# Performance work log

Hardware: AMD Instinct MI355X
Metric: run time of the kernel (lower is better)

Reference implementation:

```python
import jax, jax.numpy as jnp
import numpy as np

D_MODEL = 768
NUM_HEADS = 12


def setup_inputs() -> dict:
    key = jax.random.key(0)
    ks = jax.random.split(key, 11)
    B, N, D = 4, 2048, D_MODEL
    s = 1.0 / np.sqrt(D)
    return {
        "q": jax.random.normal(ks[0], (B, N, D), jnp.float32),
        "k": jax.random.normal(ks[1], (B, N, D), jnp.float32),
        "v": jax.random.normal(ks[2], (B, N, D), jnp.float32),
        "wq": jax.random.normal(ks[3], (D, D), jnp.float32) * s,
        "bq": jnp.zeros((D,), jnp.float32),
        "wk": jax.random.normal(ks[4], (D, D), jnp.float32) * s,
        "bk": jnp.zeros((D,), jnp.float32),
        "wv": jax.random.normal(ks[5], (D, D), jnp.float32) * s,
        "bv": jnp.zeros((D,), jnp.float32),
        "wo": jax.random.normal(ks[6], (D, D), jnp.float32) * s,
        "bo": jnp.zeros((D,), jnp.float32),
    }


def _split_heads(x, num_heads):
    B, N, D = x.shape
    hd = D // num_heads
    return x.reshape(B, N, num_heads, hd).transpose(0, 2, 1, 3)  # (B,H,N,hd)


def reference(q, k, v, wq, bq, wk, bk, wv, bv, wo, bo):
    B, N, D = q.shape
    H = NUM_HEADS
    qw = q @ wq.T + bq
    kw = k @ wk.T + bk
    vw = v @ wv.T + bv
    hq = _split_heads(qw, H)
    hk = _split_heads(kw, H)
    hv = _split_heads(vw, H)
    scale = 1.0 / jnp.sqrt(jnp.asarray(hq.shape[-1], hq.dtype))
    scores = jnp.einsum("bhnd,bhmd->bhnm", hq, hk) * scale  # (B,H,N,N) explicit
    attn = jax.nn.softmax(scores, axis=-1)
    out = jnp.einsum("bhnm,bhmd->bhnd", attn, hv)
    out = out.transpose(0, 2, 1, 3).reshape(B, N, D)
    return out @ wo.T + bo
```

## Files before the change

kernel.cpp:

```cpp
#include <hip/hip_runtime.h>
#include <hip/hip_bf16.h>
#include <type_traits>


typedef __attribute__((ext_vector_type(8)))  __bf16 bf16x8;
typedef __attribute__((ext_vector_type(4)))  __bf16 bf16x4;
typedef __attribute__((ext_vector_type(4)))  float  f32x4;
typedef __attribute__((ext_vector_type(16))) float  f32x16;
typedef __attribute__((ext_vector_type(2)))  unsigned u32x2;
typedef __attribute__((ext_vector_type(4)))  unsigned u32x4;

#define NH  12
#define HD  64
#define DM  768
#define SEQ 2048
#define NB  4
#define M8  8192
#define ALPHA 0.18033688011112043f

__device__ __forceinline__ f32x4 mfma16(bf16x8 a, bf16x8 b, f32x4 c) {
  return __builtin_amdgcn_mfma_f32_16x16x32_bf16(a, b, c, 0, 0, 0);
}
__device__ __forceinline__ f32x16 mfma32(bf16x8 a, bf16x8 b, f32x16 c) {
  return __builtin_amdgcn_mfma_f32_32x32x16_bf16(a, b, c, 0, 0, 0);
}
__device__ __forceinline__ void gload16(const void* g, void* l) {
  auto gp = (__attribute__((address_space(1))) void*)(const_cast<void*>(g));
  auto lp = (__attribute__((address_space(3))) void*)(l);
  __builtin_amdgcn_global_load_lds(gp, lp, 16, 0, 0);
}
__device__ __forceinline__ float exp2_(float x) {
#if __has_builtin(__builtin_amdgcn_exp2f)
  return __builtin_amdgcn_exp2f(x);
#else
  return exp2f(x);
#endif
}

__device__ __forceinline__ u32x2 pswap(unsigned a, unsigned b) {
#if __has_builtin(__builtin_amdgcn_permlane32_swap)
  return __builtin_amdgcn_permlane32_swap(a, b, false, false);
#else
  u32x2 r;
  unsigned sa = (unsigned)__shfl_xor((int)a, 32), sb = (unsigned)__shfl_xor((int)b, 32);
  int hi = ((int)threadIdx.x >> 5) & 1;
  r[0] = hi ? sb : a;
  r[1] = hi ? b : sa;
  return r;
#endif
}
__device__ __forceinline__ unsigned f2u(float x) { return __builtin_bit_cast(unsigned, x); }
__device__ __forceinline__ float    u2f(unsigned x) { return __builtin_bit_cast(float, x); }
__device__ __forceinline__ float pcomb_sum(float v) {
  u32x2 r = pswap(f2u(v), f2u(v));
  return u2f(r[0]) + u2f(r[1]);
}
__device__ __forceinline__ unsigned pk(float lo, float hi_) {
  unsigned short ua = __builtin_bit_cast(unsigned short, (__bf16)lo);
  unsigned short ub = __builtin_bit_cast(unsigned short, (__bf16)hi_);
  return ((unsigned)ub << 16) | ua;
}

__global__ void cast3_kernel(const float* __restrict__ a, const float* __restrict__ b,
                             const float* __restrict__ c,
                             __bf16* __restrict__ oa, __bf16* __restrict__ ob,
                             __bf16* __restrict__ oc, int n4) {
  const float* in = blockIdx.y == 0 ? a : blockIdx.y == 1 ? b : c;
  __bf16* out     = blockIdx.y == 0 ? oa : blockIdx.y == 1 ? ob : oc;
  const float sc  = blockIdx.y == 0 ? ALPHA : 1.0f;
  int i = blockIdx.x * 256 + threadIdx.x;
  if (i < n4) {
    float4 v = ((const float4*)in)[i];
    bf16x4 r;
    r[0] = (__bf16)(v.x * sc); r[1] = (__bf16)(v.y * sc);
    r[2] = (__bf16)(v.z * sc); r[3] = (__bf16)(v.w * sc);
    ((bf16x4*)out)[i] = r;
  }
}

__global__ void cast4_kernel(const float* __restrict__ a, const float* __restrict__ b,
                             const float* __restrict__ c, const float* __restrict__ d,
                             __bf16* __restrict__ oa, __bf16* __restrict__ ob,
                             __bf16* __restrict__ oc, __bf16* __restrict__ od, int n4) {
  int y = blockIdx.y;
  const float* in = y == 0 ? a : y == 1 ? b : y == 2 ? c : d;
  __bf16* out     = y == 0 ? oa : y == 1 ? ob : y == 2 ? oc : od;
  int i = blockIdx.x * 256 + threadIdx.x;
  if (i < n4) {
    float4 v = ((const float4*)in)[i];
    bf16x4 r;
    r[0] = (__bf16)v.x; r[1] = (__bf16)v.y; r[2] = (__bf16)v.z; r[3] = (__bf16)v.w;
    ((bf16x4*)out)[i] = r;
  }
}

template <typename OutT>
__device__ __forceinline__ void gemm_body(const __bf16* __restrict__ A,
                                          const __bf16* __restrict__ B,
                                          const float* __restrict__ bias,
                                          OutT* __restrict__ C,
                                          long m0, long n0, float bscale, bool trans) {
  __shared__ __align__(16) __bf16 As[128][32];
  __shared__ __align__(16) __bf16 Bs[128][32];
  const int tid = threadIdx.x;
  const int w = tid >> 6, l = tid & 63;
  const int g = l >> 4, i16 = l & 15;
  const int wr = w >> 1, wc = w & 1;
  const int srow = l >> 2;
  const int scol = (l & 3) * 8;
  f32x4 acc[4][4] = {};

  for (int k0 = 0; k0 < DM; k0 += 32) {
    __syncthreads();
#pragma unroll
    for (int s = 0; s < 2; ++s) {
      const int r0 = (s * 4 + w) * 16;
      gload16(A + (m0 + r0 + srow) * (long)DM + k0 + scol, &As[r0][0]);
      gload16(B + (n0 + r0 + srow) * (long)DM + k0 + scol, &Bs[r0][0]);
    }
    __syncthreads();
    bf16x8 af[4], bfr[4];
#pragma unroll
    for (int m = 0; m < 4; ++m) af[m] = *(const bf16x8*)&As[wr * 64 + m * 16 + i16][g * 8];
#pragma unroll
    for (int n = 0; n < 4; ++n) bfr[n] = *(const bf16x8*)&Bs[wc * 64 + n * 16 + i16][g * 8];
#pragma unroll
    for (int m = 0; m < 4; ++m)
#pragma unroll
      for (int n = 0; n < 4; ++n) acc[m][n] = mfma16(af[m], bfr[n], acc[m][n]);
  }

  if (trans) {
#pragma unroll
    for (int m = 0; m < 4; ++m)
#pragma unroll
      for (int n = 0; n < 4; ++n) {
        const long col = n0 + wc * 64 + n * 16 + i16;
        const float bv = bias[col] * bscale;
        const long row0 = m0 + wr * 64 + m * 16 + g * 4;
        bf16x4 v4;
#pragma unroll
        for (int r = 0; r < 4; ++r) v4[r] = (__bf16)(acc[m][n][r] + bv);
        *(bf16x4*)((__bf16*)C + col * (long)M8 + row0) = v4;
      }
  } else {
#pragma unroll
    for (int m = 0; m < 4; ++m)
#pragma unroll
      for (int n = 0; n < 4; ++n) {
        const long col = n0 + wc * 64 + n * 16 + i16;
        const float bv = bias[col] * bscale;
        const long row0 = m0 + wr * 64 + m * 16 + g * 4;
#pragma unroll
        for (int r = 0; r < 4; ++r) {
          const float v = acc[m][n][r] + bv;
          if constexpr (std::is_same<OutT, float>::value)
            C[(row0 + r) * DM + col] = v;
          else
            C[(row0 + r) * DM + col] = (__bf16)v;
        }
      }
  }
}

__global__ __launch_bounds__(256) void proj3_gemm(
    const __bf16* __restrict__ qb, const __bf16* __restrict__ kb, const __bf16* __restrict__ vb,
    const __bf16* __restrict__ wqb, const __bf16* __restrict__ wkb, const __bf16* __restrict__ wvb,
    const float* __restrict__ bq, const float* __restrict__ bk, const float* __restrict__ bv,
    __bf16* __restrict__ qpj, __bf16* __restrict__ kpj, __bf16* __restrict__ vpT) {
  const int gid = blockIdx.x;
  const int swz = (gid & 7) * 144 + (gid >> 3);
  const int z = swz / 384, rem = swz % 384;
  const long xb = rem / 6, yb = rem % 6;
  const __bf16* A = z == 0 ? qb : z == 1 ? kb : vb;
  const __bf16* B = z == 0 ? wqb : z == 1 ? wkb : wvb;
  const float* bias = z == 0 ? bq : z == 1 ? bk : bv;
  __bf16* C = z == 0 ? qpj : z == 1 ? kpj : vpT;
  gemm_body<__bf16>(A, B, bias, C, xb * 128, yb * 128, z == 0 ? ALPHA : 1.0f, z == 2);
}

__global__ __launch_bounds__(256) void out_gemm(const __bf16* __restrict__ A,
                                                const __bf16* __restrict__ B,
                                                const float* __restrict__ bias,
                                                float* __restrict__ C) {
  const int gid = blockIdx.x;
  const int swz = (gid & 7) * 48 + (gid >> 3);
  const long xb = swz / 6, yb = swz % 6;
  gemm_body<float>(A, B, bias, C, xb * 128, yb * 128, 1.0f, false);
}

__global__ __launch_bounds__(256) void attn_fwd(const __bf16* __restrict__ qp,
                                                const __bf16* __restrict__ kp,
                                                const __bf16* __restrict__ vpT,
                                                __bf16* __restrict__ ao) {
  __shared__ __align__(16) __bf16 Ks[2][64 * 64];
  __shared__ __align__(16) __bf16 Vs[2][64 * 64];

  const int wg = blockIdx.x;
  const int xcd = wg & 7;
  const int idx = wg >> 3;
  const int bh = xcd * 6 + (idx >> 4);
  const int qt = idx & 15;
  const int b = bh / NH, h = bh % NH;

  const int tid = threadIdx.x;
  const int w = tid >> 6, l = tid & 63;
  const int l31 = l & 31, hi = l >> 5;

  const long qrow = (long)b * SEQ + qt * 128 + w * 32 + l31;
  const __bf16* qb = qp + qrow * DM + h * HD;
  bf16x8 qf[4];
#pragma unroll
  for (int kk = 0; kk < 4; ++kk) qf[kk] = *(const bf16x8*)(qb + kk * 16 + hi * 8);

  f32x16 o0 = {}, o1 = {};
  float lsum = 0.f;

  const int srow = tid >> 3;
  const int schunk = (tid & 7) ^ (srow & 7);
  const __bf16* kbase = kp + ((long)b * SEQ) * DM + h * HD;
  const __bf16* vtb = vpT + (long)(h * HD) * M8 + (long)b * SEQ;

  auto stage = [&](int T, int sel) {
    const long kt = (long)T * 64;
    __bf16* Kd = &Ks[sel][(w * 8) * 64];
    __bf16* Vd = &Vs[sel][(w * 8) * 64];
    gload16(kbase + (kt + srow) * (long)DM + schunk * 8, Kd);
    gload16(kbase + (kt + 32 + srow) * (long)DM + schunk * 8, Kd + 32 * 64);
    gload16(vtb + (long)srow * M8 + kt + schunk * 8, Vd);
    gload16(vtb + (long)(32 + srow) * M8 + kt + schunk * 8, Vd + 32 * 64);
  };

  auto compute = [&](const __bf16* Kc, const __bf16* Vc) {
    f32x16 s0 = {}, s1 = {};
    __builtin_amdgcn_s_setprio(1);
#pragma unroll
    for (int kk = 0; kk < 4; ++kk) {
      const int cl = kk * 2 + hi;
      bf16x8 kf0 = *(const bf16x8*)&Kc[l31 * 64 + ((cl ^ (l31 & 7)) * 8)];
      s0 = mfma32(kf0, qf[kk], s0);
      bf16x8 kf1 = *(const bf16x8*)&Kc[(32 + l31) * 64 + ((cl ^ (l31 & 7)) * 8)];
      s1 = mfma32(kf1, qf[kk], s1);
    }
    __builtin_amdgcn_s_setprio(0);

#pragma unroll
    for (int r = 0; r < 16; ++r) s0[r] = exp2_(s0[r]);
#pragma unroll
    for (int r = 0; r < 16; ++r) s1[r] = exp2_(s1[r]);
    f32x16 ps = s0 + s1;
    const float t0 = (ps[0] + ps[1]) + (ps[2] + ps[3]);
    const float t1 = (ps[4] + ps[5]) + (ps[6] + ps[7]);
    const float t2 = (ps[8] + ps[9]) + (ps[10] + ps[11]);
    const float t3 = (ps[12] + ps[13]) + (ps[14] + ps[15]);
    lsum += (t0 + t1) + (t2 + t3);

    bf16x8 pf[4];
#pragma unroll
    for (int ks = 0; ks < 4; ++ks) {
      const int base = 8 * (ks & 1);
      const f32x16& S = (ks < 2) ? s0 : s1;
      unsigned pa = pk(S[base + 0], S[base + 1]);
      unsigned pc = pk(S[base + 2], S[base + 3]);
      unsigned pb = pk(S[base + 4], S[base + 5]);
      unsigned pd = pk(S[base + 6], S[base + 7]);
      u32x2 r02 = pswap(pa, pb);
      u32x2 r13 = pswap(pc, pd);
      u32x4 pw;
      pw[0] = r02[0]; pw[1] = r13[0]; pw[2] = r02[1]; pw[3] = r13[1];
      pf[ks] = __builtin_bit_cast(bf16x8, pw);
    }

    __builtin_amdgcn_s_setprio(1);
#pragma unroll
    for (int ks = 0; ks < 4; ++ks) {
      const int cl = ks * 2 + hi;
      bf16x8 vf0 = *(const bf16x8*)&Vc[l31 * 64 + ((cl ^ (l31 & 7)) * 8)];
      o0 = mfma32(vf0, pf[ks], o0);
      bf16x8 vf1 = *(const bf16x8*)&Vc[(32 + l31) * 64 + ((cl ^ (l31 & 7)) * 8)];
      o1 = mfma32(vf1, pf[ks], o1);
    }
    __builtin_amdgcn_s_setprio(0);
  };

  stage(0, 0);
  __syncthreads();
  for (int t = 0; t < SEQ / 64; t += 2) {
    if (t + 1 < SEQ / 64) stage(t + 1, 1);
    compute(Ks[0], Vs[0]);
    __syncthreads();
    if (t + 2 < SEQ / 64) stage(t + 2, 0);
    compute(Ks[1], Vs[1]);
    __syncthreads();
  }

  const float inv = 1.0f / pcomb_sum(lsum);
  __bf16* obase = ao + qrow * DM + h * HD;
#pragma unroll
  for (int rg = 0; rg < 4; ++rg) {
    bf16x4 v0, v1;
#pragma unroll
    for (int j = 0; j < 4; ++j) {
      v0[j] = (__bf16)(o0[rg * 4 + j] * inv);
      v1[j] = (__bf16)(o1[rg * 4 + j] * inv);
    }
    *(bf16x4*)(obase + 8 * rg + 4 * hi) = v0;
    *(bf16x4*)(obase + 32 + 8 * rg + 4 * hi) = v1;
  }
}

extern "C" void kernel_launch(void* const* d_in, const int* in_sizes, int n_in,
                              void* d_out, int out_size, void* d_ws, size_t ws_size,
                              hipStream_t stream) {
  const float* q  = (const float*)d_in[0];
  const float* k  = (const float*)d_in[1];
  const float* v  = (const float*)d_in[2];
  const float* wq = (const float*)d_in[3];
  const float* bq = (const float*)d_in[4];
  const float* wk = (const float*)d_in[5];
  const float* bk = (const float*)d_in[6];
  const float* wv = (const float*)d_in[7];
  const float* bv = (const float*)d_in[8];
  const float* wo = (const float*)d_in[9];
  const float* bo = (const float*)d_in[10];

  const long S = (long)M8 * DM;
  const long W = (long)DM * DM;
  __bf16* ws = (__bf16*)d_ws;
  __bf16 *qb = ws, *kb = qb + S, *vb = kb + S;
  __bf16 *wqb = vb + S, *wkb = wqb + W, *wvb = wkb + W, *wob = wvb + W;
  __bf16 *qpj = wob + W, *kpj = qpj + S, *vpT = kpj + S;
  __bf16* aob = qb;

  cast3_kernel<<<dim3((unsigned)(S / 4 / 256), 3), 256, 0, stream>>>(q, k, v, qb, kb, vb, (int)(S / 4));
  cast4_kernel<<<dim3((unsigned)(W / 4 / 256), 4), 256, 0, stream>>>(wq, wk, wv, wo, wqb, wkb, wvb, wob, (int)(W / 4));

  proj3_gemm<<<1152, 256, 0, stream>>>(qb, kb, vb, wqb, wkb, wvb, bq, bk, bv, qpj, kpj, vpT);

  attn_fwd<<<768, 256, 0, stream>>>(qpj, kpj, vpT, aob);

  out_gemm<<<384, 256, 0, stream>>>(aob, wob, bo, (float*)d_out);
}
```

Before: 168.8 us.

## Double-buffer GEMM and attention loads with explicit vmcnt waits and swizzled LDS

```diff
diff --git a/kernel.cpp b/kernel.cpp
--- a/kernel.cpp
+++ b/kernel.cpp
@@ -29,13 +29,12 @@
   auto lp = (__attribute__((address_space(3))) void*)(l);
   __builtin_amdgcn_global_load_lds(gp, lp, 16, 0, 0);
 }
-__device__ __forceinline__ float exp2_(float x) {
-#if __has_builtin(__builtin_amdgcn_exp2f)
-  return __builtin_amdgcn_exp2f(x);
-#else
-  return exp2f(x);
-#endif
-}
+__device__ __forceinline__ float exp2_(float x) { return exp2f(x); }
+
+#define VMW(n) do { asm volatile("s_waitcnt vmcnt(" #n ")" ::: "memory"); \
+                    __builtin_amdgcn_sched_barrier(0); } while (0)
+#define BARX do { __builtin_amdgcn_s_barrier(); \
+                  __builtin_amdgcn_sched_barrier(0); } while (0)
 
 __device__ __forceinline__ u32x2 pswap(unsigned a, unsigned b) {
 #if __has_builtin(__builtin_amdgcn_permlane32_swap)
@@ -100,35 +99,51 @@
                                           const float* __restrict__ bias,
                                           OutT* __restrict__ C,
                                           long m0, long n0, float bscale, bool trans) {
-  __shared__ __align__(16) __bf16 As[128][32];
-  __shared__ __align__(16) __bf16 Bs[128][32];
+  __shared__ __align__(16) char LDSG[32768];
   const int tid = threadIdx.x;
   const int w = tid >> 6, l = tid & 63;
   const int g = l >> 4, i16 = l & 15;
   const int wr = w >> 1, wc = w & 1;
   const int srow = l >> 2;
-  const int scol = (l & 3) * 8;
+  const int scol = ((l & 3) ^ ((srow >> 1) & 3)) * 8;
+  const __bf16* Ag0 = A + (m0 + 16 * w + srow) * (long)DM + scol;
+  const __bf16* Bg0 = B + (n0 + 16 * w + srow) * (long)DM + scol;
+  const int chsw = (g ^ ((i16 >> 1) & 3)) * 16;
+  const char* fA = LDSG + (wr * 64 + i16) * 64 + chsw;
+  const char* fB = LDSG + 16384 + (wc * 64 + i16) * 64 + chsw;
+
   f32x4 acc[4][4] = {};
-
-  for (int k0 = 0; k0 < DM; k0 += 32) {
-    __syncthreads();
-#pragma unroll
-    for (int s = 0; s < 2; ++s) {
-      const int r0 = (s * 4 + w) * 16;
-      gload16(A + (m0 + r0 + srow) * (long)DM + k0 + scol, &As[r0][0]);
-      gload16(B + (n0 + r0 + srow) * (long)DM + k0 + scol, &Bs[r0][0]);
-    }
-    __syncthreads();
-    bf16x8 af[4], bfr[4];
-#pragma unroll
-    for (int m = 0; m < 4; ++m) af[m] = *(const bf16x8*)&As[wr * 64 + m * 16 + i16][g * 8];
-#pragma unroll
-    for (int n = 0; n < 4; ++n) bfr[n] = *(const bf16x8*)&Bs[wc * 64 + n * 16 + i16][g * 8];
-#pragma unroll
-    for (int m = 0; m < 4; ++m)
-#pragma unroll
-      for (int n = 0; n < 4; ++n) acc[m][n] = mfma16(af[m], bfr[n], acc[m][n]);
-  }
+  int kcur = 0;
+
+#define GSTAGE(SELB) do { \
+    gload16(Ag0 + kcur, LDSG + (SELB) + w * 1024); \
+    gload16(Ag0 + 64 * (long)DM + kcur, LDSG + (SELB) + w * 1024 + 4096); \
+    gload16(Bg0 + kcur, LDSG + 16384 + (SELB) + w * 1024); \
+    gload16(Bg0 + 64 * (long)DM + kcur, LDSG + 16384 + (SELB) + w * 1024 + 4096); \
+    kcur += 32; } while (0)
+
+#define GCOMPUTE(SELB) do { \
+    bf16x8 af[4], bfr[4]; \
+    _Pragma("unroll") for (int m = 0; m < 4; ++m) \
+      af[m] = *(const bf16x8*)(fA + (SELB) + m * 1024); \
+    _Pragma("unroll") for (int n = 0; n < 4; ++n) \
+      bfr[n] = *(const bf16x8*)(fB + (SELB) + n * 1024); \
+    __builtin_amdgcn_s_setprio(1); \
+    _Pragma("unroll") for (int m = 0; m < 4; ++m) \
+      _Pragma("unroll") for (int n = 0; n < 4; ++n) \
+        acc[m][n] = mfma16(af[m], bfr[n], acc[m][n]); \
+    __builtin_amdgcn_s_setprio(0); } while (0)
+
+  GSTAGE(0); GSTAGE(8192);
+#pragma unroll 1
+  for (int k = 0; k + 128 <= DM; k += 64) {
+    VMW(4); BARX; GCOMPUTE(0);    BARX; GSTAGE(0);
+    VMW(4); BARX; GCOMPUTE(8192); BARX; GSTAGE(8192);
+  }
+  VMW(4); BARX; GCOMPUTE(0);
+  VMW(0); BARX; GCOMPUTE(8192);
+#undef GSTAGE
+#undef GCOMPUTE
 
   if (trans) {
 #pragma unroll
@@ -193,8 +208,7 @@
                                                 const __bf16* __restrict__ kp,
                                                 const __bf16* __restrict__ vpT,
                                                 __bf16* __restrict__ ao) {
-  __shared__ __align__(16) __bf16 Ks[2][64 * 64];
-  __shared__ __align__(16) __bf16 Vs[2][64 * 64];
+  __shared__ __align__(16) __bf16 KV[16384];
 
   const int wg = blockIdx.x;
   const int xcd = wg & 7;
@@ -213,86 +227,78 @@
 #pragma unroll
   for (int kk = 0; kk < 4; ++kk) qf[kk] = *(const bf16x8*)(qb + kk * 16 + hi * 8);
 
+  const char* fb[4];
+#pragma unroll
+  for (int kk = 0; kk < 4; ++kk)
+    fb[kk] = (const char*)KV + l31 * 128 + (((kk * 2 + hi) ^ (l31 & 7)) * 16);
+
   f32x16 o0 = {}, o1 = {};
   float lsum = 0.f;
 
   const int srow = tid >> 3;
   const int schunk = (tid & 7) ^ (srow & 7);
-  const __bf16* kbase = kp + ((long)b * SEQ) * DM + h * HD;
-  const __bf16* vtb = vpT + (long)(h * HD) * M8 + (long)b * SEQ;
-
-  auto stage = [&](int T, int sel) {
-    const long kt = (long)T * 64;
-    __bf16* Kd = &Ks[sel][(w * 8) * 64];
-    __bf16* Vd = &Vs[sel][(w * 8) * 64];
-    gload16(kbase + (kt + srow) * (long)DM + schunk * 8, Kd);
-    gload16(kbase + (kt + 32 + srow) * (long)DM + schunk * 8, Kd + 32 * 64);
-    gload16(vtb + (long)srow * M8 + kt + schunk * 8, Vd);
-    gload16(vtb + (long)(32 + srow) * M8 + kt + schunk * 8, Vd + 32 * 64);
-  };
-
-  auto compute = [&](const __bf16* Kc, const __bf16* Vc) {
-    f32x16 s0 = {}, s1 = {};
-    __builtin_amdgcn_s_setprio(1);
-#pragma unroll
-    for (int kk = 0; kk < 4; ++kk) {
-      const int cl = kk * 2 + hi;
-      bf16x8 kf0 = *(const bf16x8*)&Kc[l31 * 64 + ((cl ^ (l31 & 7)) * 8)];
-      s0 = mfma32(kf0, qf[kk], s0);
-      bf16x8 kf1 = *(const bf16x8*)&Kc[(32 + l31) * 64 + ((cl ^ (l31 & 7)) * 8)];
-      s1 = mfma32(kf1, qf[kk], s1);
-    }
-    __builtin_amdgcn_s_setprio(0);
-
-#pragma unroll
-    for (int r = 0; r < 16; ++r) s0[r] = exp2_(s0[r]);
-#pragma unroll
-    for (int r = 0; r < 16; ++r) s1[r] = exp2_(s1[r]);
-    f32x16 ps = s0 + s1;
-    const float t0 = (ps[0] + ps[1]) + (ps[2] + ps[3]);
-    const float t1 = (ps[4] + ps[5]) + (ps[6] + ps[7]);
-    const float t2 = (ps[8] + ps[9]) + (ps[10] + ps[11]);
-    const float t3 = (ps[12] + ps[13]) + (ps[14] + ps[15]);
-    lsum += (t0 + t1) + (t2 + t3);
-
-    bf16x8 pf[4];
-#pragma unroll
-    for (int ks = 0; ks < 4; ++ks) {
-      const int base = 8 * (ks & 1);
-      const f32x16& S = (ks < 2) ? s0 : s1;
-      unsigned pa = pk(S[base + 0], S[base + 1]);
-      unsigned pc = pk(S[base + 2], S[base + 3]);
-      unsigned pb = pk(S[base + 4], S[base + 5]);
-      unsigned pd = pk(S[base + 6], S[base + 7]);
-      u32x2 r02 = pswap(pa, pb);
-      u32x2 r13 = pswap(pc, pd);
-      u32x4 pw;
-      pw[0] = r02[0]; pw[1] = r13[0]; pw[2] = r02[1]; pw[3] = r13[1];
-      pf[ks] = __builtin_bit_cast(bf16x8, pw);
-    }
-
-    __builtin_amdgcn_s_setprio(1);
-#pragma unroll
-    for (int ks = 0; ks < 4; ++ks) {
-      const int cl = ks * 2 + hi;
-      bf16x8 vf0 = *(const bf16x8*)&Vc[l31 * 64 + ((cl ^ (l31 & 7)) * 8)];
-      o0 = mfma32(vf0, pf[ks], o0);
-      bf16x8 vf1 = *(const bf16x8*)&Vc[(32 + l31) * 64 + ((cl ^ (l31 & 7)) * 8)];
-      o1 = mfma32(vf1, pf[ks], o1);
-    }
-    __builtin_amdgcn_s_setprio(0);
-  };
-
-  stage(0, 0);
-  __syncthreads();
-  for (int t = 0; t < SEQ / 64; t += 2) {
-    if (t + 1 < SEQ / 64) stage(t + 1, 1);
-    compute(Ks[0], Vs[0]);
-    __syncthreads();
-    if (t + 2 < SEQ / 64) stage(t + 2, 0);
-    compute(Ks[1], Vs[1]);
-    __syncthreads();
-  }
+  const __bf16* kg = kp + ((long)b * SEQ + srow) * DM + h * HD + schunk * 8;
+  const __bf16* vg = vpT + ((long)(h * HD) + srow) * M8 + (long)b * SEQ + schunk * 8;
+  char* kdst = (char*)KV + w * 1024;
+
+#define ASTAGE(SELB) do { \
+    gload16(kg, kdst + (SELB)); \
+    gload16(kg + 32 * (long)DM, kdst + (SELB) + 4096); \
+    gload16(vg, kdst + 16384 + (SELB)); \
+    gload16(vg + 32 * (long)M8, kdst + 16384 + (SELB) + 4096); \
+    kg += 64 * (long)DM; vg += 64; } while (0)
+
+#define ACOMPUTE(SELB) do { \
+    f32x16 s0 = {}, s1 = {}; \
+    __builtin_amdgcn_s_setprio(1); \
+    _Pragma("unroll") for (int kk = 0; kk < 4; ++kk) { \
+      bf16x8 kf0 = *(const bf16x8*)(fb[kk] + (SELB)); \
+      s0 = mfma32(kf0, qf[kk], s0); \
+      bf16x8 kf1 = *(const bf16x8*)(fb[kk] + (SELB) + 4096); \
+      s1 = mfma32(kf1, qf[kk], s1); \
+    } \
+    __builtin_amdgcn_s_setprio(0); \
+    _Pragma("unroll") for (int r = 0; r < 16; ++r) s0[r] = exp2_(s0[r]); \
+    _Pragma("unroll") for (int r = 0; r < 16; ++r) s1[r] = exp2_(s1[r]); \
+    f32x16 ps = s0 + s1; \
+    const float t0 = (ps[0] + ps[1]) + (ps[2] + ps[3]); \
+    const float t1 = (ps[4] + ps[5]) + (ps[6] + ps[7]); \
+    const float t2 = (ps[8] + ps[9]) + (ps[10] + ps[11]); \
+    const float t3 = (ps[12] + ps[13]) + (ps[14] + ps[15]); \
+    lsum += (t0 + t1) + (t2 + t3); \
+    bf16x8 pf[4]; \
+    _Pragma("unroll") for (int ks = 0; ks < 4; ++ks) { \
+      const int base = 8 * (ks & 1); \
+      const f32x16& S = (ks < 2) ? s0 : s1; \
+      unsigned pa = pk(S[base + 0], S[base + 1]); \
+      unsigned pc = pk(S[base + 2], S[base + 3]); \
+      unsigned pb = pk(S[base + 4], S[base + 5]); \
+      unsigned pd = pk(S[base + 6], S[base + 7]); \
+      u32x2 r02 = pswap(pa, pb); \
+      u32x2 r13 = pswap(pc, pd); \
+      u32x4 pw; \
+      pw[0] = r02[0]; pw[1] = r13[0]; pw[2] = r02[1]; pw[3] = r13[1]; \
+      pf[ks] = __builtin_bit_cast(bf16x8, pw); \
+    } \
+    __builtin_amdgcn_s_setprio(1); \
+    _Pragma("unroll") for (int ks = 0; ks < 4; ++ks) { \
+      bf16x8 vf0 = *(const bf16x8*)(fb[ks] + 16384 + (SELB)); \
+      o0 = mfma32(vf0, pf[ks], o0); \
+      bf16x8 vf1 = *(const bf16x8*)(fb[ks] + 16384 + (SELB) + 4096); \
+      o1 = mfma32(vf1, pf[ks], o1); \
+    } \
+    __builtin_amdgcn_s_setprio(0); } while (0)
+
+  ASTAGE(0); ASTAGE(8192);
+#pragma unroll 1
+  for (int t = 0; t + 4 <= SEQ / 64; t += 2) {
+    VMW(4); BARX; ACOMPUTE(0);    BARX; ASTAGE(0);
+    VMW(4); BARX; ACOMPUTE(8192); BARX; ASTAGE(8192);
+  }
+  VMW(4); BARX; ACOMPUTE(0);
+  VMW(0); BARX; ACOMPUTE(8192);
+#undef ASTAGE
+#undef ACOMPUTE
 
   const float inv = 1.0f / pcomb_sum(lsum);
   __bf16* obase = ao + qrow * DM + h * HD;
```

New measurement: 189.8 us. 1.12x slower.

## Fuse fp32 activation cast into projection GEMM with double-buffered swizzled LDS

Applied to the files above, without the earlier changes.

```diff
diff --git a/kernel.cpp b/kernel.cpp
--- a/kernel.cpp
+++ b/kernel.cpp
@@ -29,13 +29,7 @@
   auto lp = (__attribute__((address_space(3))) void*)(l);
   __builtin_amdgcn_global_load_lds(gp, lp, 16, 0, 0);
 }
-__device__ __forceinline__ float exp2_(float x) {
-#if __has_builtin(__builtin_amdgcn_exp2f)
-  return __builtin_amdgcn_exp2f(x);
-#else
-  return exp2f(x);
-#endif
-}
+__device__ __forceinline__ float exp2_(float x) { return exp2f(x); }
 
 __device__ __forceinline__ u32x2 pswap(unsigned a, unsigned b) {
 #if __has_builtin(__builtin_amdgcn_permlane32_swap)
@@ -61,13 +55,14 @@
   return ((unsigned)ub << 16) | ua;
 }
 
-__global__ void cast3_kernel(const float* __restrict__ a, const float* __restrict__ b,
-                             const float* __restrict__ c,
+__global__ void cast4_kernel(const float* __restrict__ a, const float* __restrict__ b,
+                             const float* __restrict__ c, const float* __restrict__ d,
                              __bf16* __restrict__ oa, __bf16* __restrict__ ob,
-                             __bf16* __restrict__ oc, int n4) {
-  const float* in = blockIdx.y == 0 ? a : blockIdx.y == 1 ? b : c;
-  __bf16* out     = blockIdx.y == 0 ? oa : blockIdx.y == 1 ? ob : oc;
-  const float sc  = blockIdx.y == 0 ? ALPHA : 1.0f;
+                             __bf16* __restrict__ oc, __bf16* __restrict__ od, int n4) {
+  int y = blockIdx.y;
+  const float* in = y == 0 ? a : y == 1 ? b : y == 2 ? c : d;
+  __bf16* out     = y == 0 ? oa : y == 1 ? ob : y == 2 ? oc : od;
+  const float sc  = y == 0 ? ALPHA : 1.0f;
   int i = blockIdx.x * 256 + threadIdx.x;
   if (i < n4) {
     float4 v = ((const float4*)in)[i];
@@ -78,57 +73,88 @@
   }
 }
 
-__global__ void cast4_kernel(const float* __restrict__ a, const float* __restrict__ b,
-                             const float* __restrict__ c, const float* __restrict__ d,
-                             __bf16* __restrict__ oa, __bf16* __restrict__ ob,
-                             __bf16* __restrict__ oc, __bf16* __restrict__ od, int n4) {
-  int y = blockIdx.y;
-  const float* in = y == 0 ? a : y == 1 ? b : y == 2 ? c : d;
-  __bf16* out     = y == 0 ? oa : y == 1 ? ob : y == 2 ? oc : od;
-  int i = blockIdx.x * 256 + threadIdx.x;
-  if (i < n4) {
-    float4 v = ((const float4*)in)[i];
-    bf16x4 r;
-    r[0] = (__bf16)v.x; r[1] = (__bf16)v.y; r[2] = (__bf16)v.z; r[3] = (__bf16)v.w;
-    ((bf16x4*)out)[i] = r;
-  }
-}
-
-template <typename OutT>
-__device__ __forceinline__ void gemm_body(const __bf16* __restrict__ A,
+template <typename AT, typename OutT>
+__device__ __forceinline__ void gemm_body(const AT* __restrict__ A,
                                           const __bf16* __restrict__ B,
                                           const float* __restrict__ bias,
                                           OutT* __restrict__ C,
                                           long m0, long n0, float bscale, bool trans) {
-  __shared__ __align__(16) __bf16 As[128][32];
-  __shared__ __align__(16) __bf16 Bs[128][32];
+  constexpr bool AF32 = std::is_same<AT, float>::value;
+  __shared__ __align__(16) char LDSG[32768];
   const int tid = threadIdx.x;
   const int w = tid >> 6, l = tid & 63;
   const int g = l >> 4, i16 = l & 15;
   const int wr = w >> 1, wc = w & 1;
   const int srow = l >> 2;
-  const int scol = (l & 3) * 8;
+  const int kq = l & 3;
+  const int swc = kq ^ ((srow >> 1) & 3);
+
+  const __bf16* Bg = B + (n0 + 16 * w + srow) * (long)DM + swc * 8;
+  const float*  Agf = (const float*)A + (m0 + 16 * w + srow) * (long)DM + kq * 8;
+  const __bf16* Agh = (const __bf16*)A + (m0 + 16 * w + srow) * (long)DM + swc * 8;
+  char* const Awr = LDSG + w * 1024 + srow * 64 + swc * 16;
+
+  const int chsw = (g ^ ((i16 >> 1) & 3)) * 16;
+  const char* fA = LDSG + (wr * 64 + i16) * 64 + chsw;
+  const char* fB = LDSG + 16384 + (wc * 64 + i16) * 64 + chsw;
+
   f32x4 acc[4][4] = {};
-
-  for (int k0 = 0; k0 < DM; k0 += 32) {
-    __syncthreads();
-#pragma unroll
-    for (int s = 0; s < 2; ++s) {
-      const int r0 = (s * 4 + w) * 16;
-      gload16(A + (m0 + r0 + srow) * (long)DM + k0 + scol, &As[r0][0]);
-      gload16(B + (n0 + r0 + srow) * (long)DM + k0 + scol, &Bs[r0][0]);
-    }
-    __syncthreads();
-    bf16x8 af[4], bfr[4];
-#pragma unroll
-    for (int m = 0; m < 4; ++m) af[m] = *(const bf16x8*)&As[wr * 64 + m * 16 + i16][g * 8];
-#pragma unroll
-    for (int n = 0; n < 4; ++n) bfr[n] = *(const bf16x8*)&Bs[wc * 64 + n * 16 + i16][g * 8];
-#pragma unroll
-    for (int m = 0; m < 4; ++m)
-#pragma unroll
-      for (int n = 0; n < 4; ++n) acc[m][n] = mfma16(af[m], bfr[n], acc[m][n]);
-  }
+  float4 ar[4];
+  int kA = 0, kB = 0;
+
+  auto LA = [&]() {
+    if constexpr (AF32) {
+      ar[0] = *(const float4*)(Agf + kA);
+      ar[1] = *(const float4*)(Agf + kA + 4);
+      ar[2] = *(const float4*)(Agf + 64 * (long)DM + kA);
+      ar[3] = *(const float4*)(Agf + 64 * (long)DM + kA + 4);
+      kA += 32;
+    }
+  };
+  auto SB = [&](int selb) {
+    gload16(Bg + kB, LDSG + 16384 + selb + w * 1024);
+    gload16(Bg + 64 * (long)DM + kB, LDSG + 16384 + selb + w * 1024 + 4096);
+    if constexpr (!AF32) {
+      gload16(Agh + kB, LDSG + selb + w * 1024);
+      gload16(Agh + 64 * (long)DM + kB, LDSG + selb + w * 1024 + 4096);
+    }
+    kB += 32;
+  };
+  auto WA = [&](int selb) {
+    if constexpr (AF32) {
+      u32x4 u0, u1;
+      u0[0] = pk(ar[0].x, ar[0].y); u0[1] = pk(ar[0].z, ar[0].w);
+      u0[2] = pk(ar[1].x, ar[1].y); u0[3] = pk(ar[1].z, ar[1].w);
+      u1[0] = pk(ar[2].x, ar[2].y); u1[1] = pk(ar[2].z, ar[2].w);
+      u1[2] = pk(ar[3].x, ar[3].y); u1[3] = pk(ar[3].z, ar[3].w);
+      *(u32x4*)(Awr + selb) = u0;
+      *(u32x4*)(Awr + selb + 4096) = u1;
+    }
+  };
+
+#define GCOMPUTE(SELB) do { \
+    bf16x8 af[4], bfr[4]; \
+    _Pragma("unroll") for (int m = 0; m < 4; ++m) \
+      af[m] = *(const bf16x8*)(fA + (SELB) + m * 1024); \
+    _Pragma("unroll") for (int n = 0; n < 4; ++n) \
+      bfr[n] = *(const bf16x8*)(fB + (SELB) + n * 1024); \
+    __builtin_amdgcn_s_setprio(1); \
+    _Pragma("unroll") for (int m = 0; m < 4; ++m) \
+      _Pragma("unroll") for (int n = 0; n < 4; ++n) \
+        acc[m][n] = mfma16(af[m], bfr[n], acc[m][n]); \
+    __builtin_amdgcn_s_setprio(0); } while (0)
+
+  LA(); SB(0); WA(0);
+  __syncthreads();
+#pragma unroll 1
+  for (int s = 1; s + 1 < DM / 32; s += 2) {
+    LA(); SB(8192); GCOMPUTE(0);    WA(8192); __syncthreads();
+    LA(); SB(0);    GCOMPUTE(8192); WA(0);    __syncthreads();
+  }
+  LA(); SB(8192); GCOMPUTE(0); WA(8192);
+  __syncthreads();
+  GCOMPUTE(8192);
+#undef GCOMPUTE
 
   if (trans) {
 #pragma unroll
@@ -164,7 +190,7 @@
 }
 
 __global__ __launch_bounds__(256) void proj3_gemm(
-    const __bf16* __restrict__ qb, const __bf16* __restrict__ kb, const __bf16* __restrict__ vb,
+    const float* __restrict__ q, const float* __restrict__ k, const float* __restrict__ v,
     const __bf16* __restrict__ wqb, const __bf16* __restrict__ wkb, const __bf16* __restrict__ wvb,
     const float* __restrict__ bq, const float* __restrict__ bk, const float* __restrict__ bv,
     __bf16* __restrict__ qpj, __bf16* __restrict__ kpj, __bf16* __restrict__ vpT) {
@@ -172,11 +198,11 @@
   const int swz = (gid & 7) * 144 + (gid >> 3);
   const int z = swz / 384, rem = swz % 384;
   const long xb = rem / 6, yb = rem % 6;
-  const __bf16* A = z == 0 ? qb : z == 1 ? kb : vb;
+  const float* A = z == 0 ? q : z == 1 ? k : v;
   const __bf16* B = z == 0 ? wqb : z == 1 ? wkb : wvb;
   const float* bias = z == 0 ? bq : z == 1 ? bk : bv;
   __bf16* C = z == 0 ? qpj : z == 1 ? kpj : vpT;
-  gemm_body<__bf16>(A, B, bias, C, xb * 128, yb * 128, z == 0 ? ALPHA : 1.0f, z == 2);
+  gemm_body<float, __bf16>(A, B, bias, C, xb * 128, yb * 128, z == 0 ? ALPHA : 1.0f, z == 2);
 }
 
 __global__ __launch_bounds__(256) void out_gemm(const __bf16* __restrict__ A,
@@ -186,7 +212,7 @@
   const int gid = blockIdx.x;
   const int swz = (gid & 7) * 48 + (gid >> 3);
   const long xb = swz / 6, yb = swz % 6;
-  gemm_body<float>(A, B, bias, C, xb * 128, yb * 128, 1.0f, false);
+  gemm_body<__bf16, float>(A, B, bias, C, xb * 128, yb * 128, 1.0f, false);
 }
 
 __global__ __launch_bounds__(256) void attn_fwd(const __bf16* __restrict__ qp,
@@ -327,15 +353,13 @@
   const long S = (long)M8 * DM;
   const long W = (long)DM * DM;
   __bf16* ws = (__bf16*)d_ws;
-  __bf16 *qb = ws, *kb = qb + S, *vb = kb + S;
-  __bf16 *wqb = vb + S, *wkb = wqb + W, *wvb = wkb + W, *wob = wvb + W;
-  __bf16 *qpj = wob + W, *kpj = qpj + S, *vpT = kpj + S;
-  __bf16* aob = qb;
-
-  cast3_kernel<<<dim3((unsigned)(S / 4 / 256), 3), 256, 0, stream>>>(q, k, v, qb, kb, vb, (int)(S / 4));
-  cast4_kernel<<<dim3((unsigned)(W / 4 / 256), 4), 256, 0, stream>>>(wq, wk, wv, wo, wqb, wkb, wvb, wob, (int)(W / 4));
-
-  proj3_gemm<<<1152, 256, 0, stream>>>(qb, kb, vb, wqb, wkb, wvb, bq, bk, bv, qpj, kpj, vpT);
+  __bf16 *wqb = ws, *wkb = wqb + W, *wvb = wkb + W, *wob = wvb + W;
+  __bf16 *qpj = wob + W, *kpj = qpj + S, *vpT = kpj + S, *aob = vpT + S;
+
+  cast4_kernel<<<dim3((unsigned)(W / 4 / 256), 4), 256, 0, stream>>>(
+      wq, wk, wv, wo, wqb, wkb, wvb, wob, (int)(W / 4));
+
+  proj3_gemm<<<1152, 256, 0, stream>>>(q, k, v, wqb, wkb, wvb, bq, bk, bv, qpj, kpj, vpT);
 
   attn_fwd<<<768, 256, 0, stream>>>(qpj, kpj, vpT, aob);
 
```

After: 196.9 us. 1.17x slower.
